# Performance work log

Hardware: AMD Instinct MI355X
Metric: run time of the kernel (lower is better)

The kernel has to match this reference:

```python
import jax, jax.numpy as jnp
import numpy as np

# dims: batch, nodes(sensors), window, embed, topk, MLP inter width
B, NODE, WIN, EMB, TOPK, INTER = 256, 512, 64, 64, 16, 512
NEG = 0.2      # LeakyReLU negative slope in GAT attention
EPS = 1e-5     # BatchNorm eps
N = B * NODE   # total graph nodes
E = N * TOPK   # total edges


def _bn(x, gamma, beta, axes):
    # training-mode BatchNorm: batch statistics (biased var), affine gamma/beta
    m = jnp.mean(x, axis=axes, keepdims=True)
    v = jnp.var(x, axis=axes, keepdims=True)
    return (x - m) * jax.lax.rsqrt(v + EPS) * gamma + beta


def setup_inputs() -> dict:
    key = jax.random.key(0)
    ks = jax.random.split(key, 12)
    sd = lambda k, shp, s: jax.random.normal(k, shp, jnp.float32) * s
    return {
        "data": jax.random.normal(ks[0], (B, NODE, WIN), jnp.float32),
        "org_edge_index": jax.random.randint(ks[1], (2, NODE), 0, NODE, dtype=jnp.int32),  # unused by forward
        "W_emb": sd(ks[2], (NODE, EMB), 0.1),          # nn.Embedding weight
        "W_lin": sd(ks[3], (EMB, WIN), 0.1),           # GraphLayer.lin (no bias)
        "att_i": sd(ks[4], (EMB,), 0.1),
        "att_j": sd(ks[5], (EMB,), 0.1),
        "att_em_i": sd(ks[6], (EMB,), 0.1),
        "att_em_j": sd(ks[7], (EMB,), 0.1),
        "b_gnn": jnp.zeros((EMB,), jnp.float32),       # GraphLayer bias
        "g_bn1": jnp.ones((EMB,), jnp.float32), "b_bn1": jnp.zeros((EMB,), jnp.float32),
        "g_bn2": jnp.ones((EMB,), jnp.float32), "b_bn2": jnp.zeros((EMB,), jnp.float32),
        "W1": sd(ks[8], (INTER, EMB), 0.05), "b1": jnp.zeros((INTER,), jnp.float32),
        "g_bn3": jnp.ones((INTER,), jnp.float32), "b_bn3": jnp.zeros((INTER,), jnp.float32),
        "W2": sd(ks[9], (1, INTER), 0.05), "b2": jnp.zeros((1,), jnp.float32),
    }


def reference(data, org_edge_index, W_emb, W_lin, att_i, att_j, att_em_i, att_em_j,
              b_gnn, g_bn1, b_bn1, g_bn2, b_bn2, W1, b1, g_bn3, b_bn3, W2, b2):
    x = data.reshape(N, WIN)

    # ---- graph structure learning: cosine-sim top-k on DETACHED embeddings ----
    w = jax.lax.stop_gradient(W_emb)
    nw = w * jax.lax.rsqrt(jnp.sum(w * w, axis=-1, keepdims=True))
    cos = nw @ nw.T                                  # [NODE, NODE]
    _, topk_idx = jax.lax.top_k(cos, TOPK)           # [NODE, TOPK]; diag==1 -> self in top-k,
                                                     # so remove+add self-loops is a no-op on the edge set
    offs = (jnp.arange(N // NODE) * NODE)[:, None]   # batch offsets
    src = (topk_idx.reshape(-1)[None, :] + offs).reshape(-1)                 # [E] source j
    dst = (jnp.repeat(jnp.arange(NODE), TOPK)[None, :] + offs).reshape(-1)   # [E] target i (sorted)

    # ---- GAT-style message passing (heads=1, concat=False) ----
    xl = x @ W_lin.T                                 # [N, EMB]
    # per-node attention scores for key = [Wx || embedding]
    s_i = xl @ att_i + jnp.tile(W_emb @ att_em_i, B)  # [N]
    s_j = xl @ att_j + jnp.tile(W_emb @ att_em_j, B)  # [N]
    alpha = s_i[dst] + s_j[src]                      # [E]
    alpha = jnp.where(alpha > 0, alpha, NEG * alpha)  # leaky_relu
    # segment softmax over edges grouped by target node
    amax = jax.ops.segment_max(alpha, dst, num_segments=N, indices_are_sorted=True)
    ex = jnp.exp(alpha - amax[dst])
    den = jax.ops.segment_sum(ex, dst, num_segments=N, indices_are_sorted=True)
    attw = ex / den[dst]                             # [E]
    agg = jax.ops.segment_sum(attw[:, None] * xl[src], dst,
                              num_segments=N, indices_are_sorted=True)  # [N, EMB]
    h = jax.nn.relu(_bn(agg + b_gnn, g_bn1, b_bn1, axes=0))             # GNNLayer bn+relu

    # ---- readout: mul by embedding, BN over channels, MLP head (dropout=eval/identity) ----
    z = h.reshape(B, NODE, EMB) * W_emb[None]        # [B, NODE, EMB]
    z = jax.nn.relu(_bn(z, g_bn2, b_bn2, axes=(0, 1)))
    z = jax.nn.relu(_bn(z @ W1.T + b1, g_bn3, b_bn3, axes=(0, 1)))      # [B, NODE, INTER]
    out = (z @ W2.T + b2).reshape(B, NODE)
    return out
```

## Files before the change

### kernel.cpp

```cpp
#include <hip/hip_runtime.h>
#include <hip/hip_bf16.h>

constexpr int BATCH = 256, NNODE = 512, WINW = 64, EMBD = 64, KTOP = 16, CIN = 512;
constexpr int NTOT = BATCH * NNODE;
constexpr float NEGS = 0.2f;
constexpr float EPSBN = 1e-5f;
constexpr int XLP = 68;

typedef __attribute__((ext_vector_type(8))) short bf16x8;
typedef __attribute__((ext_vector_type(4))) float f32x4;

union U8 { uint4 u; bf16x8 b; };

__device__ inline float bf2f(unsigned u16) {
  union { unsigned u; float f; } v; v.u = u16 << 16; return v.f;
}
__device__ inline unsigned pkbf(float a, float b) {
  __hip_bfloat162 h = __float22bfloat162_rn(make_float2(a, b));
  return *(unsigned*)&h;
}

__global__ void k_prep(const float* __restrict__ W_emb,
                       const float* __restrict__ att_em_i,
                       const float* __restrict__ att_em_j,
                       float* __restrict__ nw, float* __restrict__ emb_si,
                       float* __restrict__ emb_sj) {
  int i = blockIdx.x, e = threadIdx.x;
  float w  = W_emb[i * EMBD + e];
  float sq = w * w;
  float si = w * att_em_i[e];
  float sj = w * att_em_j[e];
  for (int o = 32; o > 0; o >>= 1) {
    sq += __shfl_xor(sq, o);
    si += __shfl_xor(si, o);
    sj += __shfl_xor(sj, o);
  }
  nw[i * EMBD + e] = w * rsqrtf(sq);
  if (e == 0) { emb_si[i] = si; emb_sj[i] = sj; }
}

__global__ __launch_bounds__(256) void k_topk(const float* __restrict__ nw,
                                              int* __restrict__ topk) {
  __shared__ float nwi[EMBD];
  __shared__ float wbv[4];
  __shared__ int   wbi[4];
  __shared__ int   winner;
  int i = blockIdx.x, t = threadIdx.x, wv = t >> 6, ln = t & 63;
  if (t < EMBD) nwi[t] = nw[i * EMBD + t];
  __syncthreads();
  float v0 = 0.f, v1 = 0.f;
  #pragma unroll
  for (int k = 0; k < EMBD; k++) {
    v0 += nw[t * EMBD + k] * nwi[k];
    v1 += nw[(t + 256) * EMBD + k] * nwi[k];
  }
  for (int sel = 0; sel < KTOP; sel++) {
    float bv; int bi;
    if (v1 > v0) { bv = v1; bi = t + 256; } else { bv = v0; bi = t; }
    #pragma unroll
    for (int o = 1; o < 64; o <<= 1) {
      float ov = __shfl_xor(bv, o);
      int   oi = __shfl_xor(bi, o);
      if (ov > bv || (ov == bv && oi < bi)) { bv = ov; bi = oi; }
    }
    if (ln == 0) { wbv[wv] = bv; wbi[wv] = bi; }
    __syncthreads();
    if (t == 0) {
      float B = wbv[0]; int I = wbi[0];
      #pragma unroll
      for (int w = 1; w < 4; w++)
        if (wbv[w] > B || (wbv[w] == B && wbi[w] < I)) { B = wbv[w]; I = wbi[w]; }
      topk[i * KTOP + sel] = I;
      winner = I;
    }
    __syncthreads();
    int wi = winner;
    if (wi == t) v0 = -3.f;
    else if (wi == t + 256) v1 = -3.f;
  }
}

__global__ __launch_bounds__(1024) void k_fuse5(
    const float* __restrict__ data, const float* __restrict__ W_lin,
    const float* __restrict__ att_i, const float* __restrict__ att_j,
    const float* __restrict__ emb_si, const float* __restrict__ emb_sj,
    const int* __restrict__ topk,
    unsigned* __restrict__ aggb, float* __restrict__ gsum1,
    float* __restrict__ gss1) {
  __shared__ float xl[NNODE * XLP];
  __shared__ float ssi[NNODE];
  __shared__ float ssj[NNODE];
  __shared__ float ews[16][64];
  __shared__ float redb[16 * 128];
  const int b = blockIdx.x;
  const int t = threadIdx.x, w = t >> 6, ln = t & 63;
  const int lm = ln & 15, lq = ln >> 4, kb = lq * 8;

  bf16x8 bfrag[4][2];
  float ai4[4], aj4[4];
  #pragma unroll
  for (int ti = 0; ti < 4; ti++) {
    int ch = ti * 16 + lm;
    ai4[ti] = att_i[ch]; aj4[ti] = att_j[ch];
    #pragma unroll
    for (int s = 0; s < 2; s++) {
      const float* wp = W_lin + ch * WINW + s * 32 + kb;
      float4 w0 = *(const float4*)wp;
      float4 w1 = *(const float4*)(wp + 4);
      U8 f;
      f.u = make_uint4(pkbf(w0.x, w0.y), pkbf(w0.z, w0.w),
                       pkbf(w1.x, w1.y), pkbf(w1.z, w1.w));
      bfrag[ti][s] = f.b;
    }
  }
  #pragma unroll
  for (int tt = 0; tt < 2; tt++) {
    int tile = w * 2 + tt;
    const float* dr = data + ((size_t)b * NNODE + tile * 16 + lm) * WINW + kb;
    f32x4 acc[4];
    #pragma unroll
    for (int ti = 0; ti < 4; ti++) acc[ti] = (f32x4){0.f, 0.f, 0.f, 0.f};
    #pragma unroll
    for (int s = 0; s < 2; s++) {
      float4 d0 = *(const float4*)(dr + s * 32);
      float4 d1 = *(const float4*)(dr + s * 32 + 4);
      U8 af;
      af.u = make_uint4(pkbf(d0.x, d0.y), pkbf(d0.z, d0.w),
                        pkbf(d1.x, d1.y), pkbf(d1.z, d1.w));
      #pragma unroll
      for (int ti = 0; ti < 4; ti++)
        acc[ti] = __builtin_amdgcn_mfma_f32_16x16x32_bf16(af.b, bfrag[ti][s], acc[ti], 0, 0, 0);
    }
    #pragma unroll
    for (int r = 0; r < 4; r++) {
      int nd = tile * 16 + lq * 4 + r;
      float si = 0.f, sj = 0.f;
      #pragma unroll
      for (int ti = 0; ti < 4; ti++) {
        float v = acc[ti][r];
        xl[nd * XLP + ti * 16 + lm] = v;
        si += v * ai4[ti];
        sj += v * aj4[ti];
      }
      si += __shfl_xor(si, 1); si += __shfl_xor(si, 2);
      si += __shfl_xor(si, 4); si += __shfl_xor(si, 8);
      sj += __shfl_xor(sj, 1); sj += __shfl_xor(sj, 2);
      sj += __shfl_xor(sj, 4); sj += __shfl_xor(sj, 8);
      if (lm == 0) { ssi[nd] = si + emb_si[nd]; ssj[nd] = sj + emb_sj[nd]; }
    }
  }
  __syncthreads();
  const int nd4 = ln >> 4, l4 = ln & 15;
  float psx = 0.f, psy = 0.f, psz = 0.f, psw = 0.f;
  float qsx = 0.f, qsy = 0.f, qsz = 0.f, qsw = 0.f;
  for (int it = 0; it < 8; it++) {
    int node = w * 32 + it * 4 + nd4;
    const int4* tp = (const int4*)(topk + node * KTOP);
    int4 i0 = tp[0], i1 = tp[1], i2 = tp[2], i3 = tp[3];
    int idx[16] = {i0.x, i0.y, i0.z, i0.w, i1.x, i1.y, i1.z, i1.w,
                   i2.x, i2.y, i2.z, i2.w, i3.x, i3.y, i3.z, i3.w};
    float a = ssi[node] + ssj[idx[l4]];
    a = a > 0.f ? a : NEGS * a;
    float mx = a;
    mx = fmaxf(mx, __shfl_xor(mx, 1));
    mx = fmaxf(mx, __shfl_xor(mx, 2));
    mx = fmaxf(mx, __shfl_xor(mx, 4));
    mx = fmaxf(mx, __shfl_xor(mx, 8));
    float e = __expf(a - mx);
    float den = e;
    den += __shfl_xor(den, 1); den += __shfl_xor(den, 2);
    den += __shfl_xor(den, 4); den += __shfl_xor(den, 8);
    ews[w][ln] = e / den;
    float4 w0 = *(const float4*)&ews[w][nd4 * 16 + 0];
    float4 w1 = *(const float4*)&ews[w][nd4 * 16 + 4];
    float4 w2 = *(const float4*)&ews[w][nd4 * 16 + 8];
    float4 w3 = *(const float4*)&ews[w][nd4 * 16 + 12];
    float wks[16] = {w0.x, w0.y, w0.z, w0.w, w1.x, w1.y, w1.z, w1.w,
                     w2.x, w2.y, w2.z, w2.w, w3.x, w3.y, w3.z, w3.w};
    float ax = 0.f, ay = 0.f, az = 0.f, aw = 0.f;
    #pragma unroll
    for (int k = 0; k < KTOP; k++) {
      float4 v = *(const float4*)&xl[idx[k] * XLP + l4 * 4];
      ax += wks[k] * v.x; ay += wks[k] * v.y;
      az += wks[k] * v.z; aw += wks[k] * v.w;
    }
    uint2 st = make_uint2(pkbf(ax, ay), pkbf(az, aw));
    *(uint2*)(aggb + (((size_t)b * NNODE + node) << 5) + l4 * 2) = st;
    psx += ax; psy += ay; psz += az; psw += aw;
    qsx += ax * ax; qsy += ay * ay; qsz += az * az; qsw += aw * aw;
  }
  #pragma unroll
  for (int o = 16; o <= 32; o <<= 1) {
    psx += __shfl_xor(psx, o); psy += __shfl_xor(psy, o);
    psz += __shfl_xor(psz, o); psw += __shfl_xor(psw, o);
    qsx += __shfl_xor(qsx, o); qsy += __shfl_xor(qsy, o);
    qsz += __shfl_xor(qsz, o); qsw += __shfl_xor(qsw, o);
  }
  if (ln < 16) {
    float4 a = {psx, psy, psz, psw};
    float4 q = {qsx, qsy, qsz, qsw};
    *(float4*)&redb[w * 128 + ln * 4] = a;
    *(float4*)&redb[w * 128 + 64 + ln * 4] = q;
  }
  __syncthreads();
  if (t < 64) {
    float s = 0.f;
    #pragma unroll
    for (int w16 = 0; w16 < 16; w16++) s += redb[w16 * 128 + t];
    atomicAdd(&gsum1[t], s);
  } else if (t < 128) {
    int e = t - 64;
    float s = 0.f;
    #pragma unroll
    for (int w16 = 0; w16 < 16; w16++) s += redb[w16 * 128 + 64 + e];
    atomicAdd(&gss1[e], s);
  }
}

__global__ __launch_bounds__(256) void k_zstats4(
    const unsigned* __restrict__ aggb, const float* __restrict__ W_emb,
    const float* __restrict__ gsum1, const float* __restrict__ gss1,
    const float* __restrict__ g_bn1, const float* __restrict__ b_bn1,
    float* __restrict__ gsum2, float* __restrict__ gss2) {
  __shared__ float red[4][8][32];
  const float invn = 1.f / (float)NTOT;
  int t = threadIdx.x;
  int gid = blockIdx.x * 256 + t;
  int p = t & 31;
  int c0 = 2 * p;
  float m0 = gsum1[c0] * invn, vv0 = gss1[c0] * invn - m0 * m0;
  float a10 = g_bn1[c0] * rsqrtf(vv0 + EPSBN), c10 = b_bn1[c0] - m0 * a10;
  float m1 = gsum1[c0 + 1] * invn, vv1 = gss1[c0 + 1] * invn - m1 * m1;
  float a11 = g_bn1[c0 + 1] * rsqrtf(vv1 + EPSBN), c11 = b_bn1[c0 + 1] - m1 * a11;
  const float2* we2  = (const float2*)W_emb;
  float ps0 = 0.f, ps1 = 0.f, q0 = 0.f, q1 = 0.f;
  int stride = gridDim.x * 256;
  for (int idx = gid; idx < NTOT * 32; idx += stride) {
    unsigned u = aggb[idx];
    float vx = bf2f(u & 0xffffu), vy = bf2f(u >> 16);
    int node = (idx >> 5) & (NNODE - 1);
    float2 w = we2[node * 32 + p];
    float z0 = vx * a10 + c10; z0 = z0 > 0.f ? z0 : 0.f; z0 *= w.x;
    float z1 = vy * a11 + c11; z1 = z1 > 0.f ? z1 : 0.f; z1 *= w.y;
    ps0 += z0; q0 += z0 * z0; ps1 += z1; q1 += z1 * z1;
  }
  int g = t >> 5;
  red[0][g][p] = ps0; red[1][g][p] = ps1; red[2][g][p] = q0; red[3][g][p] = q1;
  __syncthreads();
  if (t < 128) {
    int v = t >> 5, p2 = t & 31;
    float s = 0.f;
    #pragma unroll
    for (int k = 0; k < 8; k++) s += red[v][k][p2];
    float* dst = (v & 2) ? gss2 : gsum2;
    atomicAdd(&dst[2 * p2 + (v & 1)], s);
  }
}

__global__ __launch_bounds__(256) void k_gram3(
    const unsigned* __restrict__ aggb, const float* __restrict__ W_emb,
    const float* __restrict__ gsum1, const float* __restrict__ gss1,
    const float* __restrict__ g_bn1, const float* __restrict__ b_bn1,
    const float* __restrict__ gsum2, const float* __restrict__ gss2,
    const float* __restrict__ g_bn2, const float* __restrict__ b_bn2,
    float* __restrict__ Gpart, float* __restrict__ hpart,
    unsigned* __restrict__ hb) {
  __shared__ float smem[4 * 4480];
  __shared__ float hred[4][64];
  const float invn = 1.f / (float)NTOT;
  const int t = threadIdx.x, wv = t >> 6, ln = t & 63;
  const int lm = ln & 15, lq = ln >> 4;
  const int r4 = ln & 7, ch8 = ln >> 3;
  const int c0 = ch8 * 8;
  float a1v[8], c1v[8], a2v[8], c2v[8];
  #pragma unroll
  for (int j = 0; j < 8; j++) {
    int ch = c0 + j;
    float m = gsum1[ch] * invn, vv = gss1[ch] * invn - m * m;
    a1v[j] = g_bn1[ch] * rsqrtf(vv + EPSBN); c1v[j] = b_bn1[ch] - m * a1v[j];
    float m2 = gsum2[ch] * invn, v2 = gss2[ch] * invn - m2 * m2;
    a2v[j] = g_bn2[ch] * rsqrtf(v2 + EPSBN); c2v[j] = b_bn2[ch] - m2 * a2v[j];
  }
  unsigned* ht = (unsigned*)(smem + wv * 4480);
  bf16x8 ones;
  #pragma unroll
  for (int j = 0; j < 8; j++) ones[j] = (short)0x3F80;
  f32x4 acc[4][4];
  f32x4 accS[4];
  #pragma unroll
  for (int i = 0; i < 4; i++) {
    accS[i] = (f32x4){0.f, 0.f, 0.f, 0.f};
    #pragma unroll
    for (int j = 0; j < 4; j++) acc[i][j] = (f32x4){0.f, 0.f, 0.f, 0.f};
  }
  const uint4* ab4 = (const uint4*)aggb;
  uint4* hb4 = (uint4*)hb;
  const float4* we4 = (const float4*)W_emb;
  const int blockrow = blockIdx.x * 256;
  #pragma unroll
  for (int ck = 0; ck < 2; ck++) {
    int k0 = blockrow + wv * 64 + ck * 32;
    #pragma unroll
    for (int rr2 = 0; rr2 < 2; rr2++) {
      float h2[2][8];
      #pragma unroll
      for (int rh = 0; rh < 2; rh++) {
        int lr = r4 * 4 + rr2 * 2 + rh;
        int row = k0 + lr;
        int node = row & (NNODE - 1);
        uint4 u = ab4[(size_t)row * 8 + ch8];
        float4 w0 = we4[node * 16 + ch8 * 2];
        float4 w1 = we4[node * 16 + ch8 * 2 + 1];
        float gv[8] = {bf2f(u.x & 0xffffu), bf2f(u.x >> 16),
                       bf2f(u.y & 0xffffu), bf2f(u.y >> 16),
                       bf2f(u.z & 0xffffu), bf2f(u.z >> 16),
                       bf2f(u.w & 0xffffu), bf2f(u.w >> 16)};
        float wv8[8] = {w0.x, w0.y, w0.z, w0.w, w1.x, w1.y, w1.z, w1.w};
        #pragma unroll
        for (int j = 0; j < 8; j++) {
          float z = gv[j] * a1v[j] + c1v[j];
          z = z > 0.f ? z : 0.f;
          z *= wv8[j];
          float hh = z * a2v[j] + c2v[j];
          hh = hh > 0.f ? hh : 0.f;
          h2[rh][j] = hh;
        }
        hb4[(size_t)row * 8 + ch8] =
            make_uint4(pkbf(h2[rh][0], h2[rh][1]), pkbf(h2[rh][2], h2[rh][3]),
                       pkbf(h2[rh][4], h2[rh][5]), pkbf(h2[rh][6], h2[rh][7]));
      }
      #pragma unroll
      for (int cc = 0; cc < 8; cc++) {
        int ch = c0 + cc;
        int base = ch * 20 + ((ch >> 3) & 3) * 4;
        ht[base + r4 * 2 + rr2] = pkbf(h2[0][cc], h2[1][cc]);
      }
    }
    bf16x8 frag[4];
    #pragma unroll
    for (int i = 0; i < 4; i++) {
      int ch = i * 16 + lm;
      int base = ch * 20 + ((ch >> 3) & 3) * 4;
      frag[i] = *(const bf16x8*)(ht + base + lq * 4);
    }
    #pragma unroll
    for (int i = 0; i < 4; i++) {
      #pragma unroll
      for (int j = 0; j < 4; j++)
        acc[i][j] = __builtin_amdgcn_mfma_f32_16x16x32_bf16(frag[i], frag[j], acc[i][j], 0, 0, 0);
      accS[i] = __builtin_amdgcn_mfma_f32_16x16x32_bf16(frag[i], ones, accS[i], 0, 0, 0);
    }
  }
  __syncthreads();
  float* Gb = smem + wv * 4480;
  #pragma unroll
  for (int i = 0; i < 4; i++) {
    #pragma unroll
    for (int j = 0; j < 4; j++) {
      float4 vv = {acc[i][j][0], acc[i][j][1], acc[i][j][2], acc[i][j][3]};
      *(float4*)(Gb + (j * 16 + lm) * 68 + i * 16 + lq * 4) = vv;
    }
    if (lm == 0) {
      float4 sv = {accS[i][0], accS[i][1], accS[i][2], accS[i][3]};
      *(float4*)&hred[wv][i * 16 + lq * 4] = sv;
    }
  }
  __syncthreads();
  for (int k = t; k < 4096; k += 256) {
    int col = k >> 6, row = k & 63;
    int o = col * 68 + row;
    Gpart[(size_t)blockIdx.x * 4096 + k] =
        smem[o] + smem[4480 + o] + smem[2 * 4480 + o] + smem[3 * 4480 + o];
  }
  if (t < 64)
    hpart[(size_t)blockIdx.x * 64 + t] =
        hred[0][t] + hred[1][t] + hred[2][t] + hred[3][t];
}

__global__ __launch_bounds__(256) void k_gred(const float* __restrict__ Gpart,
                                              const float* __restrict__ hpart,
                                              float* __restrict__ G,
                                              float* __restrict__ hsum) {
  int wi = blockIdx.x * 256 + threadIdx.x;
  if (wi < 131072) {
    int e = wi & 4095, seg = wi >> 12;
    float s = 0.f;
    #pragma unroll
    for (int k = 0; k < 16; k++) s += Gpart[(size_t)(seg * 16 + k) * 4096 + e];
    atomicAdd(&G[e], s);
  } else if (wi < 131072 + 512) {
    int wi2 = wi - 131072;
    int e = wi2 & 63, seg = wi2 >> 6;
    float s = 0.f;
    #pragma unroll 8
    for (int k = 0; k < 64; k++) s += hpart[(size_t)(seg * 64 + k) * 64 + e];
    atomicAdd(&hsum[e], s);
  }
}

__global__ __launch_bounds__(64) void k_fin3q(
    const float* __restrict__ G, const float* __restrict__ hsum,
    const float* __restrict__ W1, const float* __restrict__ b1,
    const float* __restrict__ g3, const float* __restrict__ b3,
    float* __restrict__ a3, float* __restrict__ c3) {
  __shared__ float sw[64];
  int c = blockIdx.x, i = threadIdx.x;
  float w1i = W1[c * 64 + i];
  sw[i] = w1i;
  __syncthreads();
  float gw = 0.f;
  #pragma unroll
  for (int j = 0; j < 64; j++) gw += G[j * 64 + i] * sw[j];
  float t1 = w1i * gw;
  float t2 = w1i * hsum[i];
  for (int o = 32; o > 0; o >>= 1) { t1 += __shfl_xor(t1, o); t2 += __shfl_xor(t2, o); }
  if (i == 0) {
    float b1c = b1[c];
    const float fn = (float)NTOT, invn = 1.f / fn;
    float sum3 = t2 + fn * b1c;
    float ss3  = t1 + 2.f * b1c * t2 + fn * b1c * b1c;
    float m = sum3 * invn;
    float v = ss3 * invn - m * m;
    float aa = g3[c] * rsqrtf(v + EPSBN);
    a3[c] = aa;
    c3[c] = b3[c] - m * aa;
  }
}

__global__ __launch_bounds__(512) void k_gout3(
    const unsigned* __restrict__ hb, const float* __restrict__ W1,
    const float* __restrict__ b1, const float* __restrict__ a3,
    const float* __restrict__ c3, const float* __restrict__ W2,
    const float* __restrict__ b2, float* __restrict__ out) {
  const int t = threadIdx.x, wv = t >> 6, ln = t & 63;
  const int lm = ln & 15, lq = ln >> 4, kb = lq * 8;
  bf16x8 bfrag[4][2];
  float b1c[4], a3c[4], c3c[4], w2c[4];
  #pragma unroll
  for (int nt = 0; nt < 4; nt++) {
    int col = wv * 64 + nt * 16 + lm;
    b1c[nt] = b1[col]; a3c[nt] = a3[col]; c3c[nt] = c3[col]; w2c[nt] = W2[col];
    #pragma unroll
    for (int s = 0; s < 2; s++) {
      const float* wp = W1 + col * EMBD + s * 32 + kb;
      float4 w0 = *(const float4*)wp;
      float4 w1 = *(const float4*)(wp + 4);
      U8 f;
      f.u = make_uint4(pkbf(w0.x, w0.y), pkbf(w0.z, w0.w),
                       pkbf(w1.x, w1.y), pkbf(w1.z, w1.w));
      bfrag[nt][s] = f.b;
    }
  }
  float b2v = b2[0];
  const uint4* h4 = (const uint4*)hb;
  for (int tile = blockIdx.x; tile < NTOT / 16; tile += gridDim.x) {
    int rowbase = tile * 16;
    U8 ua, ub;
    ua.u = h4[(size_t)(rowbase + lm) * 8 + lq];
    ub.u = h4[(size_t)(rowbase + lm) * 8 + 4 + lq];
    f32x4 acc[4];
    #pragma unroll
    for (int nt = 0; nt < 4; nt++) acc[nt] = (f32x4){0.f, 0.f, 0.f, 0.f};
    #pragma unroll
    for (int nt = 0; nt < 4; nt++)
      acc[nt] = __builtin_amdgcn_mfma_f32_16x16x32_bf16(ua.b, bfrag[nt][0], acc[nt], 0, 0, 0);
    #pragma unroll
    for (int nt = 0; nt < 4; nt++)
      acc[nt] = __builtin_amdgcn_mfma_f32_16x16x32_bf16(ub.b, bfrag[nt][1], acc[nt], 0, 0, 0);
    #pragma unroll
    for (int r = 0; r < 4; r++) {
      float p = 0.f;
      #pragma unroll
      for (int nt = 0; nt < 4; nt++) {
        float z2 = acc[nt][r] + b1c[nt];
        float y = z2 * a3c[nt] + c3c[nt];
        y = y > 0.f ? y : 0.f;
        p += y * w2c[nt];
      }
      p += __shfl_xor(p, 1); p += __shfl_xor(p, 2);
      p += __shfl_xor(p, 4); p += __shfl_xor(p, 8);
      if (lm == 0) {
        if (wv == 0) p += b2v;
        atomicAdd(&out[rowbase + lq * 4 + r], p);
      }
    }
  }
}

extern "C" void kernel_launch(void* const* d_in, const int* in_sizes, int n_in,
                              void* d_out, int out_size, void* d_ws, size_t ws_size,
                              hipStream_t stream) {
  const float* data     = (const float*)d_in[0];
  const float* W_emb    = (const float*)d_in[2];
  const float* W_lin    = (const float*)d_in[3];
  const float* att_i    = (const float*)d_in[4];
  const float* att_j    = (const float*)d_in[5];
  const float* att_em_i = (const float*)d_in[6];
  const float* att_em_j = (const float*)d_in[7];
  const float* g_bn1    = (const float*)d_in[9];
  const float* b_bn1    = (const float*)d_in[10];
  const float* g_bn2    = (const float*)d_in[11];
  const float* b_bn2    = (const float*)d_in[12];
  const float* W1       = (const float*)d_in[13];
  const float* b1       = (const float*)d_in[14];
  const float* g_bn3    = (const float*)d_in[15];
  const float* b_bn3    = (const float*)d_in[16];
  const float* W2       = (const float*)d_in[17];
  const float* b2       = (const float*)d_in[18];
  float* out = (float*)d_out;

  char* p = (char*)d_ws;
  auto alloc = [&](size_t bytes) {
    void* r = (void*)p;
    p += (bytes + 255) & ~(size_t)255;
    return r;
  };
  unsigned* aggb  = (unsigned*)alloc((size_t)NTOT * EMBD * 2);
  unsigned* hb    = (unsigned*)alloc((size_t)NTOT * EMBD * 2);
  float*    Gpart = (float*)alloc((size_t)512 * 4096 * 4);
  float*    hpart = (float*)alloc((size_t)512 * 64 * 4);
  float*    nw    = (float*)alloc((size_t)NNODE * EMBD * 4);
  float*    emb_si = (float*)alloc(NNODE * 4);
  float*    emb_sj = (float*)alloc(NNODE * 4);
  int*      topk   = (int*)alloc(NNODE * KTOP * 4);
  float*    stats  = (float*)alloc(4416 * 4);
  float*    coefs  = (float*)alloc(1280 * 4);

  float* gsum1 = stats;       float* gss1 = stats + 64;
  float* gsum2 = stats + 128; float* gss2 = stats + 192;
  float* G     = stats + 256; float* hsum = stats + 4352;
  float* a3 = coefs;          float* c3 = coefs + 512;

  hipMemsetAsync(stats, 0, 4416 * 4, stream);
  hipMemsetAsync(out, 0, (size_t)NTOT * 4, stream);

  k_prep<<<NNODE, 64, 0, stream>>>(W_emb, att_em_i, att_em_j, nw, emb_si, emb_sj);
  k_topk<<<NNODE, 256, 0, stream>>>(nw, topk);
  k_fuse5<<<BATCH, 1024, 0, stream>>>(data, W_lin, att_i, att_j, emb_si, emb_sj,
                                      topk, aggb, gsum1, gss1);
  k_zstats4<<<1024, 256, 0, stream>>>(aggb, W_emb, gsum1, gss1, g_bn1, b_bn1,
                                      gsum2, gss2);
  k_gram3<<<512, 256, 0, stream>>>(aggb, W_emb, gsum1, gss1, g_bn1, b_bn1,
                                   gsum2, gss2, g_bn2, b_bn2, Gpart, hpart, hb);
  k_gred<<<514, 256, 0, stream>>>(Gpart, hpart, G, hsum);
  k_fin3q<<<CIN, 64, 0, stream>>>(G, hsum, W1, b1, g_bn3, b_bn3, a3, c3);
  k_gout3<<<512, 512, 0, stream>>>(hb, W1, b1, a3, c3, W2, b2, out);
}
```

Measured before the change: 253.6 us.

## Fold memsets into kernels, single-wave top-k, vectorize z-stats loads

Removes the two hipMemsetAsync calls by zeroing the stats buffer in k_prep and the output buffer in k_topk. k_topk now stores the cosine row in shared memory and runs selection in one wavefront, with no per-iteration block barriers. The z-stats kernel switches to 16-byte loads of 8 bf16 channels per thread, with a strided shared-memory reduction. This cuts launch and sync overhead but relies on every block covering the zeroed ranges exactly (512*256 = NTOT) and on stream ordering before the atomics run.

```diff
diff --git a/kernel.cpp b/kernel.cpp
--- a/kernel.cpp
+++ b/kernel.cpp
@@ -24,8 +24,10 @@
                        const float* __restrict__ att_em_i,
                        const float* __restrict__ att_em_j,
                        float* __restrict__ nw, float* __restrict__ emb_si,
-                       float* __restrict__ emb_sj) {
+                       float* __restrict__ emb_sj, float* __restrict__ stats) {
   int i = blockIdx.x, e = threadIdx.x;
+  int gid = i * 64 + e;
+  if (gid < 4416) stats[gid] = 0.f;
   float w  = W_emb[i * EMBD + e];
   float sq = w * w;
   float si = w * att_em_i[e];
@@ -40,12 +42,12 @@
 }
 
 __global__ __launch_bounds__(256) void k_topk(const float* __restrict__ nw,
-                                              int* __restrict__ topk) {
+                                              int* __restrict__ topk,
+                                              float* __restrict__ out_zero) {
   __shared__ float nwi[EMBD];
-  __shared__ float wbv[4];
-  __shared__ int   wbi[4];
-  __shared__ int   winner;
-  int i = blockIdx.x, t = threadIdx.x, wv = t >> 6, ln = t & 63;
+  __shared__ float cosv[NNODE];
+  int i = blockIdx.x, t = threadIdx.x;
+  out_zero[i * 256 + t] = 0.f;
   if (t < EMBD) nwi[t] = nw[i * EMBD + t];
   __syncthreads();
   float v0 = 0.f, v1 = 0.f;
@@ -54,29 +56,31 @@
     v0 += nw[t * EMBD + k] * nwi[k];
     v1 += nw[(t + 256) * EMBD + k] * nwi[k];
   }
-  for (int sel = 0; sel < KTOP; sel++) {
-    float bv; int bi;
-    if (v1 > v0) { bv = v1; bi = t + 256; } else { bv = v0; bi = t; }
-    #pragma unroll
-    for (int o = 1; o < 64; o <<= 1) {
-      float ov = __shfl_xor(bv, o);
-      int   oi = __shfl_xor(bi, o);
-      if (ov > bv || (ov == bv && oi < bi)) { bv = ov; bi = oi; }
-    }
-    if (ln == 0) { wbv[wv] = bv; wbi[wv] = bi; }
-    __syncthreads();
-    if (t == 0) {
-      float B = wbv[0]; int I = wbi[0];
-      #pragma unroll
-      for (int w = 1; w < 4; w++)
-        if (wbv[w] > B || (wbv[w] == B && wbi[w] < I)) { B = wbv[w]; I = wbi[w]; }
-      topk[i * KTOP + sel] = I;
-      winner = I;
-    }
-    __syncthreads();
-    int wi = winner;
-    if (wi == t) v0 = -3.f;
-    else if (wi == t + 256) v1 = -3.f;
+  cosv[t] = v0;
+  cosv[t + 256] = v1;
+  __syncthreads();
+  if (t < 64) {
+    float vals[8];
+    #pragma unroll
+    for (int q = 0; q < 8; q++) vals[q] = cosv[t + 64 * q];
+    for (int sel = 0; sel < KTOP; sel++) {
+      float bv = vals[0]; int bq = 0;
+      #pragma unroll
+      for (int q = 1; q < 8; q++)
+        if (vals[q] > bv) { bv = vals[q]; bq = q; }
+      int bi = t + 64 * bq;
+      #pragma unroll
+      for (int o = 1; o < 64; o <<= 1) {
+        float ov = __shfl_xor(bv, o);
+        int   oi = __shfl_xor(bi, o);
+        if (ov > bv || (ov == bv && oi < bi)) { bv = ov; bi = oi; }
+      }
+      if (t == 0) topk[i * KTOP + sel] = bi;
+      int wq = bi >> 6, wl = bi & 63;
+      #pragma unroll
+      for (int q = 0; q < 8; q++)
+        if (q == wq && t == wl) vals[q] = -3.f;
+    }
   }
 }
 
@@ -217,43 +221,57 @@
   }
 }
 
-__global__ __launch_bounds__(256) void k_zstats4(
+__global__ __launch_bounds__(256) void k_zstats5(
     const unsigned* __restrict__ aggb, const float* __restrict__ W_emb,
     const float* __restrict__ gsum1, const float* __restrict__ gss1,
     const float* __restrict__ g_bn1, const float* __restrict__ b_bn1,
     float* __restrict__ gsum2, float* __restrict__ gss2) {
-  __shared__ float red[4][8][32];
+  __shared__ float sm[256 * 17];
   const float invn = 1.f / (float)NTOT;
-  int t = threadIdx.x;
-  int gid = blockIdx.x * 256 + t;
-  int p = t & 31;
-  int c0 = 2 * p;
-  float m0 = gsum1[c0] * invn, vv0 = gss1[c0] * invn - m0 * m0;
-  float a10 = g_bn1[c0] * rsqrtf(vv0 + EPSBN), c10 = b_bn1[c0] - m0 * a10;
-  float m1 = gsum1[c0 + 1] * invn, vv1 = gss1[c0 + 1] * invn - m1 * m1;
-  float a11 = g_bn1[c0 + 1] * rsqrtf(vv1 + EPSBN), c11 = b_bn1[c0 + 1] - m1 * a11;
-  const float2* we2  = (const float2*)W_emb;
-  float ps0 = 0.f, ps1 = 0.f, q0 = 0.f, q1 = 0.f;
-  int stride = gridDim.x * 256;
-  for (int idx = gid; idx < NTOT * 32; idx += stride) {
-    unsigned u = aggb[idx];
-    float vx = bf2f(u & 0xffffu), vy = bf2f(u >> 16);
-    int node = (idx >> 5) & (NNODE - 1);
-    float2 w = we2[node * 32 + p];
-    float z0 = vx * a10 + c10; z0 = z0 > 0.f ? z0 : 0.f; z0 *= w.x;
-    float z1 = vy * a11 + c11; z1 = z1 > 0.f ? z1 : 0.f; z1 *= w.y;
-    ps0 += z0; q0 += z0 * z0; ps1 += z1; q1 += z1 * z1;
-  }
-  int g = t >> 5;
-  red[0][g][p] = ps0; red[1][g][p] = ps1; red[2][g][p] = q0; red[3][g][p] = q1;
+  const int t = threadIdx.x;
+  const int gid = blockIdx.x * 256 + t;
+  const int g8 = t & 7;
+  const int c0 = g8 * 8;
+  float a1v[8], c1v[8];
+  #pragma unroll
+  for (int j = 0; j < 8; j++) {
+    int ch = c0 + j;
+    float m = gsum1[ch] * invn, vv = gss1[ch] * invn - m * m;
+    a1v[j] = g_bn1[ch] * rsqrtf(vv + EPSBN);
+    c1v[j] = b_bn1[ch] - m * a1v[j];
+  }
+  const uint4* ab4 = (const uint4*)aggb;
+  const float4* we4 = (const float4*)W_emb;
+  float s[8] = {0, 0, 0, 0, 0, 0, 0, 0}, q[8] = {0, 0, 0, 0, 0, 0, 0, 0};
+  const int stride = gridDim.x * 256;
+  for (int idx = gid; idx < NTOT * 8; idx += stride) {
+    uint4 u = ab4[idx];
+    int node = (idx >> 3) & (NNODE - 1);
+    float4 w0 = we4[node * 16 + g8 * 2];
+    float4 w1 = we4[node * 16 + g8 * 2 + 1];
+    float gv[8] = {bf2f(u.x & 0xffffu), bf2f(u.x >> 16),
+                   bf2f(u.y & 0xffffu), bf2f(u.y >> 16),
+                   bf2f(u.z & 0xffffu), bf2f(u.z >> 16),
+                   bf2f(u.w & 0xffffu), bf2f(u.w >> 16)};
+    float wv8[8] = {w0.x, w0.y, w0.z, w0.w, w1.x, w1.y, w1.z, w1.w};
+    #pragma unroll
+    for (int j = 0; j < 8; j++) {
+      float z = gv[j] * a1v[j] + c1v[j];
+      z = z > 0.f ? z : 0.f;
+      z *= wv8[j];
+      s[j] += z; q[j] += z * z;
+    }
+  }
+  #pragma unroll
+  for (int j = 0; j < 8; j++) { sm[t * 17 + j] = s[j]; sm[t * 17 + 8 + j] = q[j]; }
   __syncthreads();
   if (t < 128) {
-    int v = t >> 5, p2 = t & 31;
-    float s = 0.f;
-    #pragma unroll
-    for (int k = 0; k < 8; k++) s += red[v][k][p2];
-    float* dst = (v & 2) ? gss2 : gsum2;
-    atomicAdd(&dst[2 * p2 + (v & 1)], s);
+    int c = t & 63, st = t >> 6;
+    int col = (c & 7) + 8 * st;
+    float tot = 0.f;
+    #pragma unroll 8
+    for (int k = 0; k < 32; k++) tot += sm[((c >> 3) + 8 * k) * 17 + col];
+    atomicAdd(st ? &gss2[c] : &gsum2[c], tot);
   }
 }
 
@@ -531,14 +549,12 @@
   float* G     = stats + 256; float* hsum = stats + 4352;
   float* a3 = coefs;          float* c3 = coefs + 512;
 
-  hipMemsetAsync(stats, 0, 4416 * 4, stream);
-  hipMemsetAsync(out, 0, (size_t)NTOT * 4, stream);
-
-  k_prep<<<NNODE, 64, 0, stream>>>(W_emb, att_em_i, att_em_j, nw, emb_si, emb_sj);
-  k_topk<<<NNODE, 256, 0, stream>>>(nw, topk);
+  k_prep<<<NNODE, 64, 0, stream>>>(W_emb, att_em_i, att_em_j, nw, emb_si,
+                                   emb_sj, stats);
+  k_topk<<<NNODE, 256, 0, stream>>>(nw, topk, out);
   k_fuse5<<<BATCH, 1024, 0, stream>>>(data, W_lin, att_i, att_j, emb_si, emb_sj,
                                       topk, aggb, gsum1, gss1);
-  k_zstats4<<<1024, 256, 0, stream>>>(aggb, W_emb, gsum1, gss1, g_bn1, b_bn1,
+  k_zstats5<<<1024, 256, 0, stream>>>(aggb, W_emb, gsum1, gss1, g_bn1, b_bn1,
                                       gsum2, gss2);
   k_gram3<<<512, 256, 0, stream>>>(aggb, W_emb, gsum1, gss1, g_bn1, b_bn1,
                                    gsum2, gss2, g_bn2, b_bn2, Gpart, hpart, hb);
```

Result: faster. 247.6 us (-2.4%).
